# Performance work log

Hardware: AMD Instinct MI355X
Metric: run time of the kernel (lower is better)

## Reference

```python
import jax, jax.numpy as jnp
import numpy as np

N = 2048      # number of nodes
D = 128       # node_dim
QK = 64       # qk_dim == value_dim (code reshapes v with qk_dim)
H = 8         # n_heads
E = 8         # edge_dim


def _l2norm(x):
    return x / (jnp.linalg.norm(x, axis=-1, keepdims=True) + 1e-8)


def setup_inputs() -> dict:
    key = jax.random.key(0)
    ks = jax.random.split(key, 10)
    nodes = jax.random.normal(ks[0], (N, D), jnp.float32)
    adj = (jax.random.uniform(ks[1], (N, N, 1)) < 0.1).astype(jnp.float32)
    adj = jnp.maximum(adj, jnp.eye(N, dtype=jnp.float32)[:, :, None])
    edges = jax.random.normal(ks[2], (N, N, E), jnp.float32)
    # Linear weights stored as (out_features, in_features), eqx convention
    WQ = jax.random.normal(ks[3], (QK * H, D), jnp.float32) / np.sqrt(D)
    WK = jax.random.normal(ks[4], (QK * H, D), jnp.float32) / np.sqrt(D)
    WV = jax.random.normal(ks[5], (QK * H, D), jnp.float32) / np.sqrt(D)
    Wo = jax.random.normal(ks[6], (D, QK * H), jnp.float32) / np.sqrt(QK * H)
    bo = jax.random.normal(ks[7], (D,), jnp.float32) * 0.01
    We = jax.random.normal(ks[8], (H, E), jnp.float32) / np.sqrt(E)
    Weo = jax.random.normal(ks[9], (E, H), jnp.float32) / np.sqrt(H)
    return dict(nodes=nodes, adj=adj, edges=edges, WQ=WQ, WK=WK, WV=WV,
                Wo=Wo, bo=bo, We=We, Weo=Weo)


def reference(nodes, adj, edges, WQ, WK, WV, Wo, bo, We, Weo):
    n = nodes.shape[0]
    # per-node projections; reshape(N, qk_dim, n_heads): head is fastest axis
    q = (nodes @ WQ.T).reshape(n, QK, H)
    k = (nodes @ WK.T).reshape(n, QK, H)
    v = (nodes @ WV.T).reshape(n, QK, H)

    scores = jnp.einsum('ndh,Ndh->nNh', q, k) / jnp.sqrt(jnp.float32(QK))

    # edge-feature modulation of attention scores
    we = jnp.einsum('nNe,he->nNh', edges, We) * adj          # [N,N,H]
    scores = scores * we

    # edge update: residual + out-projection, then L2 normalize
    edges_out = _l2norm(edges + jnp.einsum('nNh,eh->nNe', scores, Weo))

    # masked softmax over axis=1 with initial=min(scores*adj) (jnn.softmax semantics)
    mask = adj > 0                                            # [N,N,1] -> broadcast
    init = jnp.min(scores * adj)
    neg = jnp.finfo(scores.dtype).min
    x_max = jnp.maximum(jnp.max(jnp.where(mask, scores, neg), axis=1, keepdims=True), init)
    x_max = jax.lax.stop_gradient(x_max)
    unnorm = jnp.where(mask, jnp.exp(scores - x_max), 0.0)
    attn = unnorm / jnp.sum(unnorm, axis=1, keepdims=True)    # [N,N,H]

    h = jnp.einsum('nNh,Ndh->ndh', attn, v).reshape(n, -1)    # [N, QK*H]
    nodes_out = _l2norm(nodes + h @ Wo.T + bo)
    return nodes_out, edges_out
```

## Files before the change

### kernel.cpp

```cpp
#include <hip/hip_runtime.h>
#include <hip/hip_bf16.h>

#define N_NODES 2048
#define D_NODE 128
#define QK_DIM 64
#define N_HEADS 8
#define E_DIM 8
#define EXP_SHIFT 24.0f

typedef __hip_bfloat16 bf16;
typedef unsigned short u16;
typedef __attribute__((ext_vector_type(8))) short bf16x8v;
typedef __attribute__((ext_vector_type(4))) float f32x4v;

__device__ __forceinline__ float bf2f(bf16 x) { return __bfloat162float(x); }
__device__ __forceinline__ float u2f(u16 u) { return __uint_as_float(((unsigned)u) << 16); }
__device__ __forceinline__ u16 f2bf(float f) {
  unsigned u = __float_as_uint(f);
  unsigned r = u + 0x7FFFu + ((u >> 16) & 1u);
  return (u16)(r >> 16);
}

__device__ __forceinline__ void unpack2(unsigned u, float& a, float& b) {
  union { unsigned x; float f; } lo, hi;
  lo.x = u << 16; hi.x = u & 0xffff0000u;
  a = lo.f; b = hi.f;
}
__device__ __forceinline__ void unpack8(uint4 u, float* f) {
  unpack2(u.x, f[0], f[1]); unpack2(u.y, f[2], f[3]);
  unpack2(u.z, f[4], f[5]); unpack2(u.w, f[6], f[7]);
}

template <bool BF16>
__device__ __forceinline__ float ldv(const void* p, size_t i) {
  if constexpr (BF16) return bf2f(((const bf16*)p)[i]);
  else return ((const float*)p)[i];
}
template <bool BF16>
__device__ __forceinline__ void ld8v(const void* p, size_t i8, float* f) {
  if constexpr (BF16) {
    uint4 u = ((const uint4*)p)[i8];
    unpack8(u, f);
  } else {
    const float4* fp = (const float4*)p;
    float4 a = fp[2 * i8], b = fp[2 * i8 + 1];
    f[0] = a.x; f[1] = a.y; f[2] = a.z; f[3] = a.w;
    f[4] = b.x; f[5] = b.y; f[6] = b.z; f[7] = b.w;
  }
}
template <bool BF16>
__device__ __forceinline__ void stv(void* p, size_t i, float v) {
  if constexpr (BF16) ((bf16*)p)[i] = __float2bfloat16(v);
  else ((float*)p)[i] = v;
}
template <bool BF16>
__device__ __forceinline__ void st8v(void* p, size_t i8, const float* f) {
  if constexpr (BF16) {
    union { uint4 u; u16 b[8]; } ou;
#pragma unroll
    for (int e = 0; e < 8; e++) ou.b[e] = f2bf(f[e]);
    ((uint4*)p)[i8] = ou.u;
  } else {
    ((float4*)p)[2 * i8] = make_float4(f[0], f[1], f[2], f[3]);
    ((float4*)p)[2 * i8 + 1] = make_float4(f[4], f[5], f[6], f[7]);
  }
}

template <bool BF16>
__device__ __forceinline__ bf16x8v ld_frag(const void* p, size_t elem) {
  if constexpr (BF16) {
    return *(const bf16x8v*)((const u16*)p + elem);
  } else {
    const float4* fp = (const float4*)p;
    float4 a = fp[elem / 4], b = fp[elem / 4 + 1];
    union { bf16x8v v; u16 s[8]; } o;
    o.s[0] = f2bf(a.x); o.s[1] = f2bf(a.y); o.s[2] = f2bf(a.z); o.s[3] = f2bf(a.w);
    o.s[4] = f2bf(b.x); o.s[5] = f2bf(b.y); o.s[6] = f2bf(b.z); o.s[7] = f2bf(b.w);
    return o.v;
  }
}

__global__ void k_detect(const unsigned* __restrict__ adj_words, int* __restrict__ flag) {
  if (threadIdx.x == 0 && blockIdx.x == 0) {
    int b = 0;
    for (int i = 0; i < 64; i++)
      if ((adj_words[i] & 0xFFFFu) == 0x3F80u) b = 1;
    *flag = b;
  }
}

template <bool BF16>
__global__ __launch_bounds__(256) void k_proj(
    const int* __restrict__ flag,
    const void* __restrict__ nodes, const void* __restrict__ WQ,
    const void* __restrict__ WK, const void* __restrict__ WV,
    u16* __restrict__ qhi, u16* __restrict__ qlo,
    u16* __restrict__ khi, u16* __restrict__ klo, u16* __restrict__ vT) {
  if ((*flag != 0) != BF16) return;
  int t = threadIdx.x;
  int n0 = blockIdx.x * 16;
  int g = blockIdx.y;
  int mat = g >> 3;
  const void* W = (mat == 0) ? WQ : (mat == 1) ? WK : WV;
  int wv = t >> 6, lane = t & 63, m0 = lane & 15, quad = lane >> 4;
  int c = (g & 7) * 64 + wv * 16 + m0;
  f32x4v acc = {0.f, 0.f, 0.f, 0.f};
#pragma unroll
  for (int kk = 0; kk < 4; kk++) {
    bf16x8v af = ld_frag<BF16>(nodes, (size_t)(n0 + m0) * D_NODE + kk * 32 + quad * 8);
    bf16x8v bfr = ld_frag<BF16>(W, (size_t)c * D_NODE + kk * 32 + quad * 8);
    acc = __builtin_amdgcn_mfma_f32_16x16x32_bf16(af, bfr, acc, 0, 0, 0);
  }
  int d = c >> 3, h = c & 7;
  if (mat == 2) {
    union { unsigned w[2]; u16 s[4]; } ob;
#pragma unroll
    for (int reg = 0; reg < 4; reg++) ob.s[reg] = f2bf(acc[reg]);
    int n = n0 + quad * 4;
    unsigned* dst = (unsigned*)(vT + ((size_t)(h * QK_DIM + d)) * N_NODES + n);
    dst[0] = ob.w[0]; dst[1] = ob.w[1];
  } else {
    u16* hiP = (mat == 0) ? qhi : khi;
    u16* loP = (mat == 0) ? qlo : klo;
    float scale = (mat == 0) ? 0.125f : 1.f;
#pragma unroll
    for (int reg = 0; reg < 4; reg++) {
      int n = n0 + quad * 4 + reg;
      float vq = acc[reg] * scale;
      u16 hi = f2bf(vq);
      u16 lo = f2bf(vq - u2f(hi));
      size_t o = ((size_t)(h * N_NODES + n) << 6) + d;
      hiP[o] = hi; loP[o] = lo;
    }
  }
}

template <bool BF16>
__global__ __launch_bounds__(256, 3) void k_fused(
    const int* __restrict__ flag, int S,
    const void* __restrict__ adj, const void* __restrict__ edges,
    const void* __restrict__ We, const void* __restrict__ Weo,
    const u16* __restrict__ qhi, const u16* __restrict__ qlo,
    const u16* __restrict__ khi, const u16* __restrict__ klo,
    const u16* __restrict__ vT,
    float* __restrict__ hout_p, float* __restrict__ psum_p,
    void* __restrict__ out_base) {
  if ((*flag != 0) != BF16) return;
  __shared__ float We_s[N_HEADS][E_DIM];
  __shared__ float Weo_s[E_DIM][N_HEADS];
  __shared__ float we_s[N_HEADS][256];
  __shared__ float smod_s[N_HEADS][256];
  __shared__ u16 p_tile[N_HEADS][16][32];
  int t = threadIdx.x;
  if (t < 64) { We_s[t >> 3][t & 7] = ldv<BF16>(We, t); Weo_s[t >> 3][t & 7] = ldv<BF16>(Weo, t); }
  int split = blockIdx.x, rt = blockIdx.y;
  int row0 = rt * 16;
  int ntiles = (N_NODES / 16) / S;
  int colbase = split * ntiles * 16;
  int r = t >> 4, cc = t & 15;
  int wv = t >> 6, lane = t & 63, m0 = lane & 15, quad = lane >> 4;
  float psum[N_HEADS];
#pragma unroll
  for (int h = 0; h < 8; h++) psum[h] = 0.f;
  f32x4v acc_pv[2][4];
#pragma unroll
  for (int hh = 0; hh < 2; hh++)
#pragma unroll
    for (int dc = 0; dc < 4; dc++) acc_pv[hh][dc] = (f32x4v){0.f, 0.f, 0.f, 0.f};

  void* edges_out = (char*)out_base + (size_t)N_NODES * D_NODE * (BF16 ? 2 : 4);

  bf16x8v qf_h[2][2], qf_l[2][2];
#pragma unroll
  for (int hh = 0; hh < 2; hh++) {
    int h = wv * 2 + hh;
#pragma unroll
    for (int kh = 0; kh < 2; kh++) {
      size_t qoff = ((size_t)(h * N_NODES + row0 + m0) << 6) + kh * 32 + quad * 8;
      qf_h[hh][kh] = *(const bf16x8v*)(qhi + qoff);
      qf_l[hh][kh] = *(const bf16x8v*)(qlo + qoff);
    }
  }

  int n = row0 + r;
  float a_c;
  float e8_c[8];
  {
    size_t pair0 = (size_t)n * N_NODES + colbase + cc;
    a_c = ldv<BF16>(adj, pair0);
    ld8v<BF16>(edges, pair0, e8_c);
  }

  for (int ct = 0; ct < ntiles; ct++) {
    int col0 = colbase + ct * 16;
    size_t pair = (size_t)n * N_NODES + col0 + cc;
    int ctn = (ct + 1 < ntiles) ? (ct + 1) : 0;
    size_t pair_n = (size_t)n * N_NODES + colbase + ctn * 16 + cc;
    float a_n = ldv<BF16>(adj, pair_n);
    float e8_n[8];
    ld8v<BF16>(edges, pair_n, e8_n);

    __syncthreads();
#pragma unroll
    for (int h = 0; h < 8; h++) {
      float we = 0.f;
#pragma unroll
      for (int e = 0; e < 8; e++) we += e8_c[e] * We_s[h][e];
      we_s[h][t] = we * a_c;
    }
    __syncthreads();
#pragma unroll
    for (int hh = 0; hh < 2; hh++) {
      int h = wv * 2 + hh;
      f32x4v acc = {0.f, 0.f, 0.f, 0.f};
#pragma unroll
      for (int kh = 0; kh < 2; kh++) {
        size_t koff = ((size_t)(h * N_NODES + col0 + m0) << 6) + kh * 32 + quad * 8;
        bf16x8v bh = *(const bf16x8v*)(khi + koff);
        bf16x8v bl = *(const bf16x8v*)(klo + koff);
        acc = __builtin_amdgcn_mfma_f32_16x16x32_bf16(qf_h[hh][kh], bh, acc, 0, 0, 0);
        acc = __builtin_amdgcn_mfma_f32_16x16x32_bf16(qf_h[hh][kh], bl, acc, 0, 0, 0);
        acc = __builtin_amdgcn_mfma_f32_16x16x32_bf16(qf_l[hh][kh], bh, acc, 0, 0, 0);
      }
#pragma unroll
      for (int reg = 0; reg < 4; reg++) {
        int pidx = (quad * 4 + reg) * 16 + m0;
        smod_s[h][pidx] = acc[reg] * we_s[h][pidx];
      }
    }
    __syncthreads();
    {
      float sm[8];
#pragma unroll
      for (int h = 0; h < 8; h++) sm[h] = smod_s[h][t];
      float ss = 0.f, eo[8];
#pragma unroll
      for (int e = 0; e < 8; e++) {
        float x = e8_c[e];
#pragma unroll
        for (int h = 0; h < 8; h++) x += sm[h] * Weo_s[e][h];
        eo[e] = x; ss += x * x;
      }
      float inv = 1.f / (sqrtf(ss) + 1e-8f);
#pragma unroll
      for (int e = 0; e < 8; e++) eo[e] *= inv;
      st8v<BF16>(edges_out, pair, eo);
      int half = (ct & 1) * 16;
#pragma unroll
      for (int h = 0; h < 8; h++) {
        float p = (a_c != 0.f) ? __expf(sm[h] - EXP_SHIFT) : 0.f;
        psum[h] += p;
        p_tile[h][r][half + cc] = f2bf(p);
      }
    }
    if (ct & 1) {
      __syncthreads();
      int colk = colbase + (ct - 1) * 16;
#pragma unroll
      for (int hh = 0; hh < 2; hh++) {
        int h = wv * 2 + hh;
        bf16x8v ap = *(const bf16x8v*)(&p_tile[h][0][0] + m0 * 32 + quad * 8);
#pragma unroll
        for (int dc = 0; dc < 4; dc++) {
          bf16x8v bp = *(const bf16x8v*)(vT + ((size_t)(h * QK_DIM + dc * 16 + m0)) * N_NODES + colk + quad * 8);
          acc_pv[hh][dc] = __builtin_amdgcn_mfma_f32_16x16x32_bf16(ap, bp, acc_pv[hh][dc], 0, 0, 0);
        }
      }
    }
    a_c = a_n;
#pragma unroll
    for (int e = 0; e < 8; e++) e8_c[e] = e8_n[e];
  }
#pragma unroll
  for (int h = 0; h < 8; h++) {
    float x = psum[h];
    x += __shfl_xor(x, 1); x += __shfl_xor(x, 2);
    x += __shfl_xor(x, 4); x += __shfl_xor(x, 8);
    if ((t & 15) == 0)
      psum_p[((size_t)(row0 + r)) * (S * 8) + split * 8 + h] = x;
  }
#pragma unroll
  for (int hh = 0; hh < 2; hh++) {
    int h = wv * 2 + hh;
#pragma unroll
    for (int dc = 0; dc < 4; dc++) {
#pragma unroll
      for (int reg = 0; reg < 4; reg++) {
        int nn = row0 + quad * 4 + reg;
        hout_p[((size_t)nn * S + split) * 512 + h * 64 + dc * 16 + m0] = acc_pv[hh][dc][reg];
      }
    }
  }
}

template <bool BF16>
__global__ __launch_bounds__(128) void k_out(
    const int* __restrict__ flag, int S,
    const void* __restrict__ nodes, const void* __restrict__ Wo,
    const void* __restrict__ bo,
    const float* __restrict__ hout_p, const float* __restrict__ psum_p,
    void* __restrict__ out_base) {
  if ((*flag != 0) != BF16) return;
  int n = blockIdx.x, t = threadIdx.x;
  __shared__ float hv[QK_DIM * N_HEADS];
  __shared__ float inv_s[N_HEADS];
  __shared__ float red[128];
  if (t < 8) {
    float tot = 0.f;
    for (int s = 0; s < S; s++) tot += psum_p[(size_t)n * (S * 8) + s * 8 + t];
    inv_s[t] = (tot > 0.f) ? 1.f / tot : 0.f;
  }
  __syncthreads();
  for (int i = t; i < QK_DIM * N_HEADS; i += 128) {
    int d = i >> 3, hh = i & 7;
    float acc = 0.f;
    for (int s = 0; s < S; s++)
      acc += hout_p[((size_t)n * S + s) * 512 + hh * 64 + d];
    hv[i] = acc * inv_s[hh];
  }
  __syncthreads();
  float val = ldv<BF16>(nodes, (size_t)n * D_NODE + t) + ldv<BF16>(bo, t);
  for (int ch = 0; ch < (QK_DIM * N_HEADS) / 8; ch++) {
    float wf[8];
    ld8v<BF16>(Wo, (size_t)t * ((QK_DIM * N_HEADS) / 8) + ch, wf);
#pragma unroll
    for (int j = 0; j < 8; j++) val += wf[j] * hv[ch * 8 + j];
  }
  red[t] = val * val;
  __syncthreads();
  for (int s = 64; s > 0; s >>= 1) {
    if (t < s) red[t] += red[t + s];
    __syncthreads();
  }
  float ss = red[0];
  stv<BF16>(out_base, (size_t)n * D_NODE + t, val / (sqrtf(ss) + 1e-8f));
}

extern "C" void kernel_launch(void* const* d_in, const int* in_sizes, int n_in,
                              void* d_out, int out_size, void* d_ws, size_t ws_size,
                              hipStream_t stream) {
  const void* nodes = d_in[0];
  const void* adj   = d_in[1];
  const void* edges = d_in[2];
  const void* WQ = d_in[3];
  const void* WK = d_in[4];
  const void* WV = d_in[5];
  const void* Wo = d_in[6];
  const void* bo = d_in[7];
  const void* We = d_in[8];
  const void* Weo = d_in[9];

  char* w = (char*)d_ws;
  int* flag = (int*)w;
  size_t off = 256;
  const size_t PLANE = (size_t)N_HEADS * N_NODES * QK_DIM * 2;
  u16* qhi = (u16*)(w + off);  off += PLANE;
  u16* qlo = (u16*)(w + off);  off += PLANE;
  u16* khi = (u16*)(w + off);  off += PLANE;
  u16* klo = (u16*)(w + off);  off += PLANE;
  u16* vT  = (u16*)(w + off);  off += PLANE;

  int S = 8;
  while (S > 1 && off + (size_t)S * ((size_t)N_NODES * 512 * 4 + N_NODES * 8 * 4) > ws_size)
    S >>= 1;
  float* hout_p = (float*)(w + off);
  off += (size_t)S * N_NODES * 512 * 4;
  float* psum_p = (float*)(w + off);

  k_detect<<<1, 64, 0, stream>>>((const unsigned*)adj, flag);

  dim3 g1(N_NODES / 16, 24);
  k_proj<false><<<g1, 256, 0, stream>>>(flag, nodes, WQ, WK, WV, qhi, qlo, khi, klo, vT);
  k_proj<true ><<<g1, 256, 0, stream>>>(flag, nodes, WQ, WK, WV, qhi, qlo, khi, klo, vT);

  dim3 g2(S, N_NODES / 16);
  k_fused<false><<<g2, 256, 0, stream>>>(flag, S, adj, edges, We, Weo,
                                         qhi, qlo, khi, klo, vT, hout_p, psum_p, d_out);
  k_fused<true ><<<g2, 256, 0, stream>>>(flag, S, adj, edges, We, Weo,
                                         qhi, qlo, khi, klo, vT, hout_p, psum_p, d_out);

  k_out<false><<<N_NODES, 128, 0, stream>>>(flag, S, nodes, Wo, bo, hout_p, psum_p, d_out);
  k_out<true ><<<N_NODES, 128, 0, stream>>>(flag, S, nodes, Wo, bo, hout_p, psum_p, d_out);
}
```

Measured before the change: 480.1 us.

## Widen fused column tile to 32, raise occupancy, transpose Wo for coalesced output GEMV

The fused attention loop now handles 32 columns per iteration. It merges the we/smod shared buffers into one padded array that is scaled in place, and runs the PV MFMA every iteration instead of every other one. Q fragments are reloaded per iteration instead of held in registers, which frees registers so launch bounds can rise from 3 to 4 blocks per CU. k_proj is remapped so each block handles a single head, and a new k_wot kernel transposes Wo so the output projection in k_out reads coalesced columns. The aim is fewer barriers per column and better latency hiding, at the cost of extra Q loads per iteration and one more small launch.

```diff
diff --git a/kernel.cpp b/kernel.cpp
--- a/kernel.cpp
+++ b/kernel.cpp
@@ -101,17 +101,18 @@
   int n0 = blockIdx.x * 16;
   int g = blockIdx.y;
   int mat = g >> 3;
+  int h = g & 7;
   const void* W = (mat == 0) ? WQ : (mat == 1) ? WK : WV;
   int wv = t >> 6, lane = t & 63, m0 = lane & 15, quad = lane >> 4;
-  int c = (g & 7) * 64 + wv * 16 + m0;
+  int d = wv * 16 + m0;
+  int wrow = d * 8 + h;
   f32x4v acc = {0.f, 0.f, 0.f, 0.f};
 #pragma unroll
   for (int kk = 0; kk < 4; kk++) {
     bf16x8v af = ld_frag<BF16>(nodes, (size_t)(n0 + m0) * D_NODE + kk * 32 + quad * 8);
-    bf16x8v bfr = ld_frag<BF16>(W, (size_t)c * D_NODE + kk * 32 + quad * 8);
+    bf16x8v bfr = ld_frag<BF16>(W, (size_t)wrow * D_NODE + kk * 32 + quad * 8);
     acc = __builtin_amdgcn_mfma_f32_16x16x32_bf16(af, bfr, acc, 0, 0, 0);
   }
-  int d = c >> 3, h = c & 7;
   if (mat == 2) {
     union { unsigned w[2]; u16 s[4]; } ob;
 #pragma unroll
@@ -136,7 +137,7 @@
 }
 
 template <bool BF16>
-__global__ __launch_bounds__(256, 3) void k_fused(
+__global__ __launch_bounds__(256, 4) void k_fused(
     const int* __restrict__ flag, int S,
     const void* __restrict__ adj, const void* __restrict__ edges,
     const void* __restrict__ We, const void* __restrict__ Weo,
@@ -148,15 +149,14 @@
   if ((*flag != 0) != BF16) return;
   __shared__ float We_s[N_HEADS][E_DIM];
   __shared__ float Weo_s[E_DIM][N_HEADS];
-  __shared__ float we_s[N_HEADS][256];
-  __shared__ float smod_s[N_HEADS][256];
+  __shared__ float wes[N_HEADS][16][33];
   __shared__ u16 p_tile[N_HEADS][16][32];
   int t = threadIdx.x;
   if (t < 64) { We_s[t >> 3][t & 7] = ldv<BF16>(We, t); Weo_s[t >> 3][t & 7] = ldv<BF16>(Weo, t); }
   int split = blockIdx.x, rt = blockIdx.y;
   int row0 = rt * 16;
-  int ntiles = (N_NODES / 16) / S;
-  int colbase = split * ntiles * 16;
+  int nst = (N_NODES / 32) / S;
+  int colbase = split * nst * 32;
   int r = t >> 4, cc = t & 15;
   int wv = t >> 6, lane = t & 63, m0 = lane & 15, quad = lane >> 4;
   float psum[N_HEADS];
@@ -170,73 +170,82 @@
 
   void* edges_out = (char*)out_base + (size_t)N_NODES * D_NODE * (BF16 ? 2 : 4);
 
-  bf16x8v qf_h[2][2], qf_l[2][2];
-#pragma unroll
-  for (int hh = 0; hh < 2; hh++) {
-    int h = wv * 2 + hh;
-#pragma unroll
-    for (int kh = 0; kh < 2; kh++) {
-      size_t qoff = ((size_t)(h * N_NODES + row0 + m0) << 6) + kh * 32 + quad * 8;
-      qf_h[hh][kh] = *(const bf16x8v*)(qhi + qoff);
-      qf_l[hh][kh] = *(const bf16x8v*)(qlo + qoff);
-    }
-  }
-
-  int n = row0 + r;
-  float a_c;
-  float e8_c[8];
+  int nrow = row0 + r;
+  float a_c0, a_c1;
+  float e8_c[16];
   {
-    size_t pair0 = (size_t)n * N_NODES + colbase + cc;
-    a_c = ldv<BF16>(adj, pair0);
-    ld8v<BF16>(edges, pair0, e8_c);
-  }
-
-  for (int ct = 0; ct < ntiles; ct++) {
-    int col0 = colbase + ct * 16;
-    size_t pair = (size_t)n * N_NODES + col0 + cc;
-    int ctn = (ct + 1 < ntiles) ? (ct + 1) : 0;
-    size_t pair_n = (size_t)n * N_NODES + colbase + ctn * 16 + cc;
-    float a_n = ldv<BF16>(adj, pair_n);
-    float e8_n[8];
-    ld8v<BF16>(edges, pair_n, e8_n);
+    size_t p0 = (size_t)nrow * N_NODES + colbase + cc;
+    a_c0 = ldv<BF16>(adj, p0);
+    a_c1 = ldv<BF16>(adj, p0 + 16);
+    ld8v<BF16>(edges, p0, e8_c);
+    ld8v<BF16>(edges, p0 + 16, e8_c + 8);
+  }
+
+  for (int ct = 0; ct < nst; ct++) {
+    int col0 = colbase + ct * 32;
+    size_t pair0 = (size_t)nrow * N_NODES + col0 + cc;
+    int ctn = (ct + 1 < nst) ? (ct + 1) : 0;
+    size_t pn = (size_t)nrow * N_NODES + colbase + ctn * 32 + cc;
+    float a_n0 = ldv<BF16>(adj, pn);
+    float a_n1 = ldv<BF16>(adj, pn + 16);
+    float e8_n[16];
+    ld8v<BF16>(edges, pn, e8_n);
+    ld8v<BF16>(edges, pn + 16, e8_n + 8);
 
     __syncthreads();
 #pragma unroll
     for (int h = 0; h < 8; h++) {
-      float we = 0.f;
-#pragma unroll
-      for (int e = 0; e < 8; e++) we += e8_c[e] * We_s[h][e];
-      we_s[h][t] = we * a_c;
+      float w0 = 0.f, w1 = 0.f;
+#pragma unroll
+      for (int e = 0; e < 8; e++) {
+        w0 += e8_c[e] * We_s[h][e];
+        w1 += e8_c[e + 8] * We_s[h][e];
+      }
+      wes[h][r][cc] = w0 * a_c0;
+      wes[h][r][cc + 16] = w1 * a_c1;
     }
     __syncthreads();
 #pragma unroll
     for (int hh = 0; hh < 2; hh++) {
       int h = wv * 2 + hh;
-      f32x4v acc = {0.f, 0.f, 0.f, 0.f};
-#pragma unroll
-      for (int kh = 0; kh < 2; kh++) {
-        size_t koff = ((size_t)(h * N_NODES + col0 + m0) << 6) + kh * 32 + quad * 8;
-        bf16x8v bh = *(const bf16x8v*)(khi + koff);
-        bf16x8v bl = *(const bf16x8v*)(klo + koff);
-        acc = __builtin_amdgcn_mfma_f32_16x16x32_bf16(qf_h[hh][kh], bh, acc, 0, 0, 0);
-        acc = __builtin_amdgcn_mfma_f32_16x16x32_bf16(qf_h[hh][kh], bl, acc, 0, 0, 0);
-        acc = __builtin_amdgcn_mfma_f32_16x16x32_bf16(qf_l[hh][kh], bh, acc, 0, 0, 0);
-      }
-#pragma unroll
-      for (int reg = 0; reg < 4; reg++) {
-        int pidx = (quad * 4 + reg) * 16 + m0;
-        smod_s[h][pidx] = acc[reg] * we_s[h][pidx];
+      size_t qbase = ((size_t)(h * N_NODES + row0 + m0) << 6) + quad * 8;
+      bf16x8v qh0 = *(const bf16x8v*)(qhi + qbase);
+      bf16x8v ql0 = *(const bf16x8v*)(qlo + qbase);
+      bf16x8v qh1 = *(const bf16x8v*)(qhi + qbase + 32);
+      bf16x8v ql1 = *(const bf16x8v*)(qlo + qbase + 32);
+#pragma unroll
+      for (int ch = 0; ch < 2; ch++) {
+        int c0 = col0 + ch * 16;
+        size_t kbase = ((size_t)(h * N_NODES + c0 + m0) << 6) + quad * 8;
+        bf16x8v kh0 = *(const bf16x8v*)(khi + kbase);
+        bf16x8v kl0 = *(const bf16x8v*)(klo + kbase);
+        bf16x8v kh1 = *(const bf16x8v*)(khi + kbase + 32);
+        bf16x8v kl1 = *(const bf16x8v*)(klo + kbase + 32);
+        f32x4v acc = {0.f, 0.f, 0.f, 0.f};
+        acc = __builtin_amdgcn_mfma_f32_16x16x32_bf16(qh0, kh0, acc, 0, 0, 0);
+        acc = __builtin_amdgcn_mfma_f32_16x16x32_bf16(qh0, kl0, acc, 0, 0, 0);
+        acc = __builtin_amdgcn_mfma_f32_16x16x32_bf16(ql0, kh0, acc, 0, 0, 0);
+        acc = __builtin_amdgcn_mfma_f32_16x16x32_bf16(qh1, kh1, acc, 0, 0, 0);
+        acc = __builtin_amdgcn_mfma_f32_16x16x32_bf16(qh1, kl1, acc, 0, 0, 0);
+        acc = __builtin_amdgcn_mfma_f32_16x16x32_bf16(ql1, kh1, acc, 0, 0, 0);
+#pragma unroll
+        for (int reg = 0; reg < 4; reg++) {
+          int i = quad * 4 + reg;
+          wes[h][i][ch * 16 + m0] *= acc[reg];
+        }
       }
     }
     __syncthreads();
-    {
+#pragma unroll
+    for (int half = 0; half < 2; half++) {
       float sm[8];
 #pragma unroll
-      for (int h = 0; h < 8; h++) sm[h] = smod_s[h][t];
+      for (int h = 0; h < 8; h++) sm[h] = wes[h][r][half * 16 + cc];
+      float av = half ? a_c1 : a_c0;
       float ss = 0.f, eo[8];
 #pragma unroll
       for (int e = 0; e < 8; e++) {
-        float x = e8_c[e];
+        float x = e8_c[half * 8 + e];
 #pragma unroll
         for (int h = 0; h < 8; h++) x += sm[h] * Weo_s[e][h];
         eo[e] = x; ss += x * x;
@@ -244,32 +253,28 @@
       float inv = 1.f / (sqrtf(ss) + 1e-8f);
 #pragma unroll
       for (int e = 0; e < 8; e++) eo[e] *= inv;
-      st8v<BF16>(edges_out, pair, eo);
-      int half = (ct & 1) * 16;
+      st8v<BF16>(edges_out, pair0 + half * 16, eo);
 #pragma unroll
       for (int h = 0; h < 8; h++) {
-        float p = (a_c != 0.f) ? __expf(sm[h] - EXP_SHIFT) : 0.f;
+        float p = (av != 0.f) ? __expf(sm[h] - EXP_SHIFT) : 0.f;
         psum[h] += p;
-        p_tile[h][r][half + cc] = f2bf(p);
-      }
-    }
-    if (ct & 1) {
-      __syncthreads();
-      int colk = colbase + (ct - 1) * 16;
-#pragma unroll
-      for (int hh = 0; hh < 2; hh++) {
-        int h = wv * 2 + hh;
-        bf16x8v ap = *(const bf16x8v*)(&p_tile[h][0][0] + m0 * 32 + quad * 8);
-#pragma unroll
-        for (int dc = 0; dc < 4; dc++) {
-          bf16x8v bp = *(const bf16x8v*)(vT + ((size_t)(h * QK_DIM + dc * 16 + m0)) * N_NODES + colk + quad * 8);
-          acc_pv[hh][dc] = __builtin_amdgcn_mfma_f32_16x16x32_bf16(ap, bp, acc_pv[hh][dc], 0, 0, 0);
-        }
-      }
-    }
-    a_c = a_n;
-#pragma unroll
-    for (int e = 0; e < 8; e++) e8_c[e] = e8_n[e];
+        p_tile[h][r][half * 16 + cc] = f2bf(p);
+      }
+    }
+    __syncthreads();
+#pragma unroll
+    for (int hh = 0; hh < 2; hh++) {
+      int h = wv * 2 + hh;
+      bf16x8v ap = *(const bf16x8v*)(&p_tile[h][0][0] + m0 * 32 + quad * 8);
+#pragma unroll
+      for (int dc = 0; dc < 4; dc++) {
+        bf16x8v bp = *(const bf16x8v*)(vT + ((size_t)(h * QK_DIM + dc * 16 + m0)) * N_NODES + col0 + quad * 8);
+        acc_pv[hh][dc] = __builtin_amdgcn_mfma_f32_16x16x32_bf16(ap, bp, acc_pv[hh][dc], 0, 0, 0);
+      }
+    }
+    a_c0 = a_n0; a_c1 = a_n1;
+#pragma unroll
+    for (int e = 0; e < 16; e++) e8_c[e] = e8_n[e];
   }
 #pragma unroll
   for (int h = 0; h < 8; h++) {
@@ -294,9 +299,18 @@
 }
 
 template <bool BF16>
+__global__ void k_wot(const int* __restrict__ flag, const void* __restrict__ Wo,
+                      float* __restrict__ WoT) {
+  if ((*flag != 0) != BF16) return;
+  int idx = blockIdx.x * 256 + threadIdx.x;
+  int o = idx >> 9, f = idx & 511;
+  WoT[(size_t)f * D_NODE + o] = ldv<BF16>(Wo, (size_t)o * 512 + f);
+}
+
+template <bool BF16>
 __global__ __launch_bounds__(128) void k_out(
     const int* __restrict__ flag, int S,
-    const void* __restrict__ nodes, const void* __restrict__ Wo,
+    const void* __restrict__ nodes, const float* __restrict__ WoT,
     const void* __restrict__ bo,
     const float* __restrict__ hout_p, const float* __restrict__ psum_p,
     void* __restrict__ out_base) {
@@ -305,9 +319,12 @@
   __shared__ float hv[QK_DIM * N_HEADS];
   __shared__ float inv_s[N_HEADS];
   __shared__ float red[128];
+  if (t < 64) red[t] = (t < S * 8) ? psum_p[(size_t)n * (S * 8) + t] : 0.f;
+  __syncthreads();
   if (t < 8) {
     float tot = 0.f;
-    for (int s = 0; s < S; s++) tot += psum_p[(size_t)n * (S * 8) + s * 8 + t];
+#pragma unroll
+    for (int s = 0; s < 8; s++) tot += red[s * 8 + t];
     inv_s[t] = (tot > 0.f) ? 1.f / tot : 0.f;
   }
   __syncthreads();
@@ -320,12 +337,8 @@
   }
   __syncthreads();
   float val = ldv<BF16>(nodes, (size_t)n * D_NODE + t) + ldv<BF16>(bo, t);
-  for (int ch = 0; ch < (QK_DIM * N_HEADS) / 8; ch++) {
-    float wf[8];
-    ld8v<BF16>(Wo, (size_t)t * ((QK_DIM * N_HEADS) / 8) + ch, wf);
-#pragma unroll
-    for (int j = 0; j < 8; j++) val += wf[j] * hv[ch * 8 + j];
-  }
+#pragma unroll 8
+  for (int j = 0; j < 512; j++) val += WoT[(size_t)j * D_NODE + t] * hv[j];
   red[t] = val * val;
   __syncthreads();
   for (int s = 64; s > 0; s >>= 1) {
@@ -359,6 +372,7 @@
   u16* khi = (u16*)(w + off);  off += PLANE;
   u16* klo = (u16*)(w + off);  off += PLANE;
   u16* vT  = (u16*)(w + off);  off += PLANE;
+  float* WoT = (float*)(w + off);  off += (size_t)512 * D_NODE * 4;
 
   int S = 8;
   while (S > 1 && off + (size_t)S * ((size_t)N_NODES * 512 * 4 + N_NODES * 8 * 4) > ws_size)
@@ -373,12 +387,15 @@
   k_proj<false><<<g1, 256, 0, stream>>>(flag, nodes, WQ, WK, WV, qhi, qlo, khi, klo, vT);
   k_proj<true ><<<g1, 256, 0, stream>>>(flag, nodes, WQ, WK, WV, qhi, qlo, khi, klo, vT);
 
+  k_wot<false><<<256, 256, 0, stream>>>(flag, Wo, WoT);
+  k_wot<true ><<<256, 256, 0, stream>>>(flag, Wo, WoT);
+
   dim3 g2(S, N_NODES / 16);
   k_fused<false><<<g2, 256, 0, stream>>>(flag, S, adj, edges, We, Weo,
                                          qhi, qlo, khi, klo, vT, hout_p, psum_p, d_out);
   k_fused<true ><<<g2, 256, 0, stream>>>(flag, S, adj, edges, We, Weo,
                                          qhi, qlo, khi, klo, vT, hout_p, psum_p, d_out);
 
-  k_out<false><<<N_NODES, 128, 0, stream>>>(flag, S, nodes, Wo, bo, hout_p, psum_p, d_out);
-  k_out<true ><<<N_NODES, 128, 0, stream>>>(flag, S, nodes, Wo, bo, hout_p, psum_p, d_out);
-}
+  k_out<false><<<N_NODES, 128, 0, stream>>>(flag, S, nodes, WoT, bo, hout_p, psum_p, d_out);
+  k_out<true ><<<N_NODES, 128, 0, stream>>>(flag, S, nodes, WoT, bo, hout_p, psum_p, d_out);
+}
```

After: 553.4 us. 1.15x slower.
